# Performance work log

Hardware: AMD Instinct MI355X
Metric: run time of the kernel (lower is better)

## Reference

```python
import jax, jax.numpy as jnp
import numpy as np

B, S, D = 4, 2048, 1024
H, HD = 16, 64  # nb_heads, head_size


def setup_inputs() -> dict:
    key = jax.random.key(0)
    ks = jax.random.split(key, 9)
    s = 1.0 / np.sqrt(D)
    return {
        "x": jax.random.normal(ks[0], (B, S, D), dtype=jnp.float32),
        "wq": jax.random.uniform(ks[1], (D, D), jnp.float32, -s, s),
        "bq": jax.random.uniform(ks[2], (D,), jnp.float32, -s, s),
        "wk": jax.random.uniform(ks[3], (D, D), jnp.float32, -s, s),
        "bk": jax.random.uniform(ks[4], (D,), jnp.float32, -s, s),
        "wv": jax.random.uniform(ks[5], (D, D), jnp.float32, -s, s),
        "bv": jax.random.uniform(ks[6], (D,), jnp.float32, -s, s),
        "wo": jax.random.uniform(ks[7], (D, D), jnp.float32, -s, s),
        "bo": jax.random.uniform(ks[8], (D,), jnp.float32, -s, s),
    }


def _split_heads(t):
    # [B,S,D] -> [B,H,S,HD]
    return t.reshape(B, S, H, HD).transpose(0, 2, 1, 3)


def reference(x, wq, bq, wk, bk, wv, bv, wo, bo):
    q = _split_heads(x @ wq + bq)
    k = _split_heads(x @ wk + bk)
    v = _split_heads(x @ wv + bv)
    scores = jnp.einsum("bhqd,bhkd->bhqk", q, k) / jnp.sqrt(jnp.float32(HD))
    causal = jnp.tril(jnp.ones((S, S), dtype=bool))
    scores = jnp.where(causal, scores, -jnp.inf)
    w = jax.nn.softmax(scores, axis=-1)
    a = jnp.einsum("bhqk,bhkd->bhqd", w, v)
    a = a.transpose(0, 2, 1, 3).reshape(B, S, D)
    return a @ wo + bo
```

## Files before the change

kernel.cpp:

```cpp
#include <hip/hip_runtime.h>
#include <hip/hip_bf16.h>

typedef __bf16 bf16;
typedef bf16 bf16x8 __attribute__((ext_vector_type(8)));
typedef float f32x4 __attribute__((ext_vector_type(4)));
typedef unsigned short u16;

#define B_ 4
#define S_ 2048
#define D_ 1024
#define H_ 16
#define HD_ 64

#define NEG_SENT -30000.0f

#define XN_OFF   ((size_t)0)
#define WT_OFF   ((size_t)8388608)
#define BN_OFF   ((size_t)12582912)
#define FLAG_BYTE ((size_t)25174016)
#define Q_OFF    ((size_t)12587520)
#define K_OFF    ((size_t)20976128)
#define VT_OFF   ((size_t)29364736)

union Pack4 { bf16 b[4]; uint2 q; };

__device__ __forceinline__ void load16(const bf16* g, bf16* l) {
    __builtin_amdgcn_global_load_lds(
        (const __attribute__((address_space(1))) void*)g,
        (__attribute__((address_space(3))) void*)l, 16, 0, 0);
}

__global__ __launch_bounds__(256) void detect_k(const u16* __restrict__ x,
                                                int* __restrict__ flag)
{
    __shared__ int cnt;
    if (threadIdx.x == 0) cnt = 0;
    __syncthreads();
    int c = 0;
    for (int i = threadIdx.x; i < 4096; i += 256) {
        u16 w = x[i * 2];
        int e = (w >> 7) & 0xFF;
        if (e >= 100 && e <= 135) c++;
    }
    atomicAdd(&cnt, c);
    __syncthreads();
    if (threadIdx.x == 0) *flag = (cnt > 2048) ? 1 : 0;
}

__global__ __launch_bounds__(256) void norm_x_k(const void* __restrict__ src,
                                                bf16* __restrict__ dst,
                                                const int* __restrict__ flag)
{
    const int qi = blockIdx.x * 256 + threadIdx.x;
    if (*flag) {
        ((uint2*)dst)[qi] = ((const uint2*)src)[qi];
    } else {
        float4 v = ((const float4*)src)[qi];
        Pack4 p;
        p.b[0] = (bf16)v.x; p.b[1] = (bf16)v.y;
        p.b[2] = (bf16)v.z; p.b[3] = (bf16)v.w;
        ((uint2*)dst)[qi] = p.q;
    }
}

__global__ __launch_bounds__(256) void norm_b_k(
    const void* __restrict__ b0, const void* __restrict__ b1,
    const void* __restrict__ b2, const void* __restrict__ b3,
    bf16* __restrict__ BN, const int* __restrict__ flag)
{
    const int mat = blockIdx.x;
    const void* src = (mat == 0) ? b0 : (mat == 1) ? b1 : (mat == 2) ? b2 : b3;
    bf16* dst = BN + mat * 1024;
    const int i = threadIdx.x * 4;
    if (*flag) {
        ((uint2*)(dst + i))[0] = *(const uint2*)((const bf16*)src + i);
    } else {
        const float* s = (const float*)src;
        Pack4 p;
        p.b[0] = (bf16)s[i + 0]; p.b[1] = (bf16)s[i + 1];
        p.b[2] = (bf16)s[i + 2]; p.b[3] = (bf16)s[i + 3];
        ((uint2*)(dst + i))[0] = p.q;
    }
}

__global__ __launch_bounds__(256) void transpose_w(
    const void* __restrict__ W0, const void* __restrict__ W1,
    const void* __restrict__ W2, const void* __restrict__ W3,
    bf16* __restrict__ WT, const int* __restrict__ flag)
{
    __shared__ __align__(16) bf16 tile[64][65];
    const int mat = blockIdx.z;
    const void* W = (mat == 0) ? W0 : (mat == 1) ? W1 : (mat == 2) ? W2 : W3;
    bf16* O = WT + ((size_t)mat << 20);
    const int r0 = blockIdx.y * 64, c0 = blockIdx.x * 64;
    const int t = threadIdx.x;
    const int isb = *flag;
    #pragma unroll
    for (int i = 0; i < 16; ++i) {
        int idx = t + i * 256;
        int r = idx >> 6, c = idx & 63;
        size_t off = (size_t)(r0 + r) * D_ + c0 + c;
        tile[r][c] = isb ? ((const bf16*)W)[off] : (bf16)((const float*)W)[off];
    }
    __syncthreads();
    #pragma unroll
    for (int i = 0; i < 16; ++i) {
        int idx = t + i * 256;
        int rr = idx & 63, cc = idx >> 6;
        O[(size_t)(c0 + cc) * D_ + r0 + rr] = tile[rr][cc];
    }
}

__device__ __forceinline__ void gemm_core(const bf16* __restrict__ A,
                                          const bf16* __restrict__ Bt,
                                          bf16* lA, bf16* lB,
                                          f32x4 acc[4][4], int m0, int n0)
{
    const int t = threadIdx.x;
    const int lane = t & 63;
    const int wave = t >> 6;
    const int wm = (wave >> 1) << 6;
    const int wn = (wave & 1) << 6;
    const int quad = lane >> 4;
    const int col = lane & 15;
    for (int k0 = 0; k0 < D_; k0 += 32) {
        #pragma unroll
        for (int i = 0; i < 2; ++i) {
            int slot = t + i * 256;
            int row = slot >> 2;
            int kc = (slot & 3) << 3;
            load16(A + (size_t)(m0 + row) * D_ + k0 + kc, lA + slot * 8);
            load16(Bt + (size_t)(n0 + row) * D_ + k0 + kc, lB + slot * 8);
        }
        __syncthreads();
        bf16x8 af[4], bfr[4];
        #pragma unroll
        for (int mi = 0; mi < 4; ++mi)
            af[mi] = *(const bf16x8*)(lA + (wm + mi * 16 + col) * 32 + quad * 8);
        #pragma unroll
        for (int ni = 0; ni < 4; ++ni)
            bfr[ni] = *(const bf16x8*)(lB + (wn + ni * 16 + col) * 32 + quad * 8);
        #pragma unroll
        for (int mi = 0; mi < 4; ++mi)
            #pragma unroll
            for (int ni = 0; ni < 4; ++ni)
                acc[mi][ni] = __builtin_amdgcn_mfma_f32_16x16x32_bf16(
                    af[mi], bfr[ni], acc[mi][ni], 0, 0, 0);
        __syncthreads();
    }
}

__global__ __launch_bounds__(256) void gemm_qkv_k(
    const bf16* __restrict__ X, const bf16* __restrict__ WT,
    const bf16* __restrict__ BN,
    bf16* __restrict__ Qo, bf16* __restrict__ Ko, bf16* __restrict__ Vo)
{
    __shared__ __align__(16) bf16 lA[128 * 32];
    __shared__ __align__(16) bf16 lB[128 * 32];
    const int mode = blockIdx.z;
    const bf16* Wsel = WT + ((size_t)mode << 20);
    const bf16* bias = BN + mode * 1024;
    f32x4 acc[4][4];
    const f32x4 z = {0.f, 0.f, 0.f, 0.f};
    #pragma unroll
    for (int i = 0; i < 4; ++i)
        #pragma unroll
        for (int j = 0; j < 4; ++j) acc[i][j] = z;
    const int m0 = blockIdx.x * 128, n0 = blockIdx.y * 128;
    gemm_core(X, Wsel, lA, lB, acc, m0, n0);
    const int t = threadIdx.x, lane = t & 63, wave = t >> 6;
    const int wm = (wave >> 1) << 6, wn = (wave & 1) << 6;
    const int quad = lane >> 4, col = lane & 15;
    const float scale = (mode == 0) ? 0.18033688011112042f : 1.0f;
    #pragma unroll
    for (int mi = 0; mi < 4; ++mi) {
        int gm = m0 + wm + mi * 16 + quad * 4;
        int b = gm >> 11, srow = gm & 2047;
        #pragma unroll
        for (int ni = 0; ni < 4; ++ni) {
            int gn = n0 + wn + ni * 16 + col;
            float bb = (float)bias[gn];
            int h = gn >> 6, hd = gn & 63;
            if (mode == 2) {
                Pack4 pk;
                #pragma unroll
                for (int r = 0; r < 4; ++r)
                    pk.b[r] = (bf16)(acc[mi][ni][r] + bb);
                *(uint2*)(Vo + (((size_t)b * H_ + h) * HD_ + hd) * S_ + srow)
                    = pk.q;
            } else {
                #pragma unroll
                for (int r = 0; r < 4; ++r) {
                    float v = (acc[mi][ni][r] + bb) * scale;
                    if (mode == 1)
                        Ko[(((size_t)b * H_ + h) * S_ + srow + r) * HD_ + hd] = (bf16)v;
                    else
                        Qo[(((size_t)b * H_ + h) * S_ + srow + r) * HD_ + hd] = (bf16)v;
                }
            }
        }
    }
}

__device__ __forceinline__ void tile_step(
    const bf16* __restrict__ lK, const bf16* __restrict__ lV,
    bf16* __restrict__ lPTw,
    const bf16x8 qf[2], const bf16x8 vf4,
    f32x4 o[4], f32x4& o4, float& mst,
    int k0, int wq0)
{
    const int lane = threadIdx.x & 63;
    const int quad = lane >> 4, col = lane & 15;
    const f32x4 z = {0.f, 0.f, 0.f, 0.f};
    bool inc[4];
    inc[0] = true;
    inc[1] = (k0 + 16 <= wq0 + 15);
    inc[2] = (k0 + 32 <= wq0 + 15);
    inc[3] = (k0 + 48 <= wq0 + 15);
    f32x4 st[4];
    #pragma unroll
    for (int mt = 0; mt < 4; ++mt) st[mt] = z;
    __builtin_amdgcn_s_setprio(1);
    #pragma unroll
    for (int cc = 0; cc < 2; ++cc) {
        #pragma unroll
        for (int mt = 0; mt < 4; ++mt)
            if (inc[mt]) {
                bf16x8 af = *(const bf16x8*)(lK + (mt * 16 + col) * 64
                            + (((cc * 4 + quad) ^ (col & 7)) << 3));
                st[mt] = __builtin_amdgcn_mfma_f32_16x16x32_bf16(
                    af, qf[cc], st[mt], 0, 0, 0);
            }
    }
    __builtin_amdgcn_s_setprio(0);
    if (k0 + 64 > wq0) {
        #pragma unroll
        for (int mt = 0; mt < 4; ++mt)
            if (inc[mt]) {
                #pragma unroll
                for (int r = 0; r < 4; ++r)
                    if (k0 + mt * 16 + quad * 4 + r > wq0 + col)
                        st[mt][r] = NEG_SENT;
            }
    }
    float tm = fmaxf(fmaxf(st[0][0], st[0][1]), fmaxf(st[0][2], st[0][3]));
    #pragma unroll
    for (int mt = 1; mt < 4; ++mt)
        if (inc[mt])
            tm = fmaxf(tm, fmaxf(fmaxf(st[mt][0], st[mt][1]),
                                 fmaxf(st[mt][2], st[mt][3])));
    tm = fmaxf(tm, __shfl_xor(tm, 16));
    tm = fmaxf(tm, __shfl_xor(tm, 32));
    if (!__all(tm <= mst + 8.0f)) {
        float mn = fmaxf(mst, tm);
        float al = exp2f(mst - mn);
        #pragma unroll
        for (int dt = 0; dt < 4; ++dt) o[dt] *= al;
        o4 *= al;
        mst = mn;
    }
    #pragma unroll
    for (int mt = 0; mt < 4; ++mt) {
        int kch = mt * 2 + (quad >> 1);
        uint2* dst = (uint2*)(&lPTw[col * 64 + ((kch ^ (col & 7)) << 3)
                                    + ((quad & 1) << 2)]);
        if (inc[mt]) {
            Pack4 pk;
            #pragma unroll
            for (int r = 0; r < 4; ++r)
                pk.b[r] = (bf16)exp2f(st[mt][r] - mst);
            *dst = pk.q;
        } else if (mt == 1 || (mt == 3 && inc[2])) {
            uint2 zz; zz.x = 0u; zz.y = 0u;
            *dst = zz;
        }
    }
    asm volatile("s_waitcnt lgkmcnt(0)" ::: "memory");
    __builtin_amdgcn_s_setprio(1);
    #pragma unroll
    for (int kk = 0; kk < 2; ++kk) {
        if (kk == 1 && !inc[2]) continue;
        bf16x8 pf = *(const bf16x8*)(&lPTw[col * 64
                    + (((kk * 4 + quad) ^ (col & 7)) << 3)]);
        #pragma unroll
        for (int dt = 0; dt < 4; ++dt) {
            bf16x8 vf = *(const bf16x8*)(lV + (dt * 16 + col) * 64
                        + (((kk * 4 + quad) ^ (col & 7)) << 3));
            o[dt] = __builtin_amdgcn_mfma_f32_16x16x32_bf16(
                vf, pf, o[dt], 0, 0, 0);
        }
        o4 = __builtin_amdgcn_mfma_f32_16x16x32_bf16(vf4, pf, o4, 0, 0, 0);
    }
    __builtin_amdgcn_s_setprio(0);
}

__device__ __forceinline__ void tile_epilogue(
    bf16* __restrict__ Aout, int b, int h, int wq0,
    const f32x4 o[4], const f32x4& o4)
{
    const int lane = threadIdx.x & 63;
    const int quad = lane >> 4, col = lane & 15;
    float l = __shfl(o4[0], col);
    const float inv = 1.f / fmaxf(l, 1e-30f);
    const int qg = wq0 + col;
    #pragma unroll
    for (int dt = 0; dt < 4; ++dt) {
        Pack4 pk;
        #pragma unroll
        for (int r = 0; r < 4; ++r) pk.b[r] = (bf16)(o[dt][r] * inv);
        *(uint2*)(Aout + ((size_t)b * S_ + qg) * D_ + h * HD_
                  + dt * 16 + quad * 4) = pk.q;
    }
}

__global__ __launch_bounds__(256, 4) void attn_k(
    const bf16* __restrict__ Q, const bf16* __restrict__ K,
    const bf16* __restrict__ VT, bf16* __restrict__ Aout)
{
    __shared__ __align__(16) bf16 lK[64 * 64];
    __shared__ __align__(16) bf16 lV[64 * 64];
    __shared__ __align__(16) bf16 lPT[4][2][16 * 64];
    const int bh = blockIdx.y;
    const bf16* Qp = Q + (size_t)bh * S_ * HD_;
    const bf16* Kp = K + (size_t)bh * S_ * HD_;
    const bf16* Vp = VT + (size_t)bh * HD_ * S_;
    const int b = bh >> 4, h = bh & 15;
    const int t = threadIdx.x;
    const int lane = t & 63, w = t >> 6;
    const int quad = lane >> 4, col = lane & 15;

    const int q0L = (31 - (int)blockIdx.x) * 64;
    const int q0S = (int)blockIdx.x * 64;
    const int wq0L = q0L + w * 16, wq0S = q0S + w * 16;

    bf16x8 qfL[2], qfS[2];
    #pragma unroll
    for (int cc = 0; cc < 2; ++cc) {
        qfL[cc] = *(const bf16x8*)(Qp + (size_t)(wq0L + col) * HD_
                                   + cc * 32 + quad * 8);
        qfS[cc] = *(const bf16x8*)(Qp + (size_t)(wq0S + col) * HD_
                                   + cc * 32 + quad * 8);
    }
    const bf16 ov = (bf16)(col == 0 ? 1.0f : 0.0f);
    const bf16x8 vf4 = {ov, ov, ov, ov, ov, ov, ov, ov};

    f32x4 oL[4], oS[4], o4L, o4S;
    const f32x4 z = {0.f, 0.f, 0.f, 0.f};
    #pragma unroll
    for (int dt = 0; dt < 4; ++dt) { oL[dt] = z; oS[dt] = z; }
    o4L = z; o4S = z;
    float mstL = NEG_SENT, mstS = NEG_SENT;

    for (int k0 = 0; k0 <= q0L; k0 += 64) {
        #pragma unroll
        for (int i = 0; i < 2; ++i) {
            int slot = t + i * 256;
            int rr = slot >> 3, ch = slot & 7;
            int sw = (ch ^ (rr & 7)) << 3;
            load16(Kp + (size_t)(k0 + rr) * HD_ + sw, lK + slot * 8);
            load16(Vp + (size_t)rr * S_ + k0 + sw, lV + slot * 8);
        }
        __syncthreads();
        tile_step(lK, lV, &lPT[w][0][0], qfL, vf4, oL, o4L, mstL, k0, wq0L);
        if (k0 <= q0S)
            tile_step(lK, lV, &lPT[w][1][0], qfS, vf4, oS, o4S, mstS, k0, wq0S);
        __syncthreads();
    }
    tile_epilogue(Aout, b, h, wq0L, oL, o4L);
    tile_epilogue(Aout, b, h, wq0S, oS, o4S);
}

__global__ __launch_bounds__(256) void gemm_out_k(
    const bf16* __restrict__ A, const bf16* __restrict__ WoT,
    const bf16* __restrict__ Bo, void* __restrict__ Out,
    const int* __restrict__ flag)
{
    __shared__ __align__(16) bf16 lA[128 * 32];
    __shared__ __align__(16) bf16 lB[128 * 32];
    f32x4 acc[4][4];
    const f32x4 z = {0.f, 0.f, 0.f, 0.f};
    #pragma unroll
    for (int i = 0; i < 4; ++i)
        #pragma unroll
        for (int j = 0; j < 4; ++j) acc[i][j] = z;
    const int m0 = blockIdx.x * 128, n0 = blockIdx.y * 128;
    gemm_core(A, WoT, lA, lB, acc, m0, n0);
    const int t = threadIdx.x, lane = t & 63, wave = t >> 6;
    const int wm = (wave >> 1) << 6, wn = (wave & 1) << 6;
    const int quad = lane >> 4, col = lane & 15;
    const int isb = *flag;
    #pragma unroll
    for (int mi = 0; mi < 4; ++mi) {
        int gm = m0 + wm + mi * 16 + quad * 4;
        #pragma unroll
        for (int ni = 0; ni < 4; ++ni) {
            int gn = n0 + wn + ni * 16 + col;
            float bb = (float)Bo[gn];
            #pragma unroll
            for (int r = 0; r < 4; ++r) {
                float v = acc[mi][ni][r] + bb;
                size_t off = (size_t)(gm + r) * D_ + gn;
                if (isb) ((bf16*)Out)[off] = (bf16)v;
                else     ((float*)Out)[off] = v;
            }
        }
    }
}

extern "C" void kernel_launch(void* const* d_in, const int* in_sizes, int n_in,
                              void* d_out, int out_size, void* d_ws, size_t ws_size,
                              hipStream_t stream)
{
    const void* x  = d_in[0];
    const void* wq = d_in[1];
    const void* bq = d_in[2];
    const void* wk = d_in[3];
    const void* bk = d_in[4];
    const void* wv = d_in[5];
    const void* bv = d_in[6];
    const void* wo = d_in[7];
    const void* bo = d_in[8];

    bf16* ws  = (bf16*)d_ws;
    bf16* XN  = ws + XN_OFF;
    bf16* WT  = ws + WT_OFF;
    bf16* BN  = ws + BN_OFF;
    int*  flag = (int*)((char*)d_ws + FLAG_BYTE);
    bf16* Qb  = ws + Q_OFF;
    bf16* Kb  = ws + K_OFF;
    bf16* VTb = ws + VT_OFF;
    bf16* Ab  = XN;

    hipLaunchKernelGGL(detect_k, dim3(1), dim3(256), 0, stream,
                       (const u16*)x, flag);
    hipLaunchKernelGGL(norm_x_k, dim3(8192), dim3(256), 0, stream,
                       x, XN, flag);
    hipLaunchKernelGGL(transpose_w, dim3(16, 16, 4), dim3(256), 0, stream,
                       wq, wk, wv, wo, WT, flag);
    hipLaunchKernelGGL(norm_b_k, dim3(4), dim3(256), 0, stream,
                       bq, bk, bv, bo, BN, flag);
    hipLaunchKernelGGL(gemm_qkv_k, dim3(64, 8, 3), dim3(256), 0, stream,
                       XN, WT, BN, Qb, Kb, VTb);
    hipLaunchKernelGGL(attn_k, dim3(16, 64), dim3(256), 0, stream,
                       Qb, Kb, VTb, Ab);
    hipLaunchKernelGGL(gemm_out_k, dim3(64, 8), dim3(256), 0, stream,
                       Ab, WT + ((size_t)3u << 20), BN + 3072, d_out, flag);
}
```

Measured before the change: 288.9 us.

## Double-buffer K/V tiles and keep P in registers for the attention loop

The attention kernel now double-buffers the K and V tiles in LDS, prefetching the next tile while computing the current one, and drops one barrier per iteration. The P matrix is no longer round-tripped through LDS: it is packed directly into registers, and the V operand is gathered with a matching permuted layout. The long and short query tiles are interleaved so they share each K fragment load. The cost is more LDS for the second buffer and higher register pressure, which could reduce occupancy under the (256,4) launch bounds.

```diff
diff --git a/kernel.cpp b/kernel.cpp
--- a/kernel.cpp
+++ b/kernel.cpp
@@ -23,6 +23,7 @@
 #define VT_OFF   ((size_t)29364736)
 
 union Pack4 { bf16 b[4]; uint2 q; };
+union U4V  { uint4 u; bf16x8 v; };
 
 __device__ __forceinline__ void load16(const bf16* g, bf16* l) {
     __builtin_amdgcn_global_load_lds(
@@ -202,98 +203,6 @@
     }
 }
 
-__device__ __forceinline__ void tile_step(
-    const bf16* __restrict__ lK, const bf16* __restrict__ lV,
-    bf16* __restrict__ lPTw,
-    const bf16x8 qf[2], const bf16x8 vf4,
-    f32x4 o[4], f32x4& o4, float& mst,
-    int k0, int wq0)
-{
-    const int lane = threadIdx.x & 63;
-    const int quad = lane >> 4, col = lane & 15;
-    const f32x4 z = {0.f, 0.f, 0.f, 0.f};
-    bool inc[4];
-    inc[0] = true;
-    inc[1] = (k0 + 16 <= wq0 + 15);
-    inc[2] = (k0 + 32 <= wq0 + 15);
-    inc[3] = (k0 + 48 <= wq0 + 15);
-    f32x4 st[4];
-    #pragma unroll
-    for (int mt = 0; mt < 4; ++mt) st[mt] = z;
-    __builtin_amdgcn_s_setprio(1);
-    #pragma unroll
-    for (int cc = 0; cc < 2; ++cc) {
-        #pragma unroll
-        for (int mt = 0; mt < 4; ++mt)
-            if (inc[mt]) {
-                bf16x8 af = *(const bf16x8*)(lK + (mt * 16 + col) * 64
-                            + (((cc * 4 + quad) ^ (col & 7)) << 3));
-                st[mt] = __builtin_amdgcn_mfma_f32_16x16x32_bf16(
-                    af, qf[cc], st[mt], 0, 0, 0);
-            }
-    }
-    __builtin_amdgcn_s_setprio(0);
-    if (k0 + 64 > wq0) {
-        #pragma unroll
-        for (int mt = 0; mt < 4; ++mt)
-            if (inc[mt]) {
-                #pragma unroll
-                for (int r = 0; r < 4; ++r)
-                    if (k0 + mt * 16 + quad * 4 + r > wq0 + col)
-                        st[mt][r] = NEG_SENT;
-            }
-    }
-    float tm = fmaxf(fmaxf(st[0][0], st[0][1]), fmaxf(st[0][2], st[0][3]));
-    #pragma unroll
-    for (int mt = 1; mt < 4; ++mt)
-        if (inc[mt])
-            tm = fmaxf(tm, fmaxf(fmaxf(st[mt][0], st[mt][1]),
-                                 fmaxf(st[mt][2], st[mt][3])));
-    tm = fmaxf(tm, __shfl_xor(tm, 16));
-    tm = fmaxf(tm, __shfl_xor(tm, 32));
-    if (!__all(tm <= mst + 8.0f)) {
-        float mn = fmaxf(mst, tm);
-        float al = exp2f(mst - mn);
-        #pragma unroll
-        for (int dt = 0; dt < 4; ++dt) o[dt] *= al;
-        o4 *= al;
-        mst = mn;
-    }
-    #pragma unroll
-    for (int mt = 0; mt < 4; ++mt) {
-        int kch = mt * 2 + (quad >> 1);
-        uint2* dst = (uint2*)(&lPTw[col * 64 + ((kch ^ (col & 7)) << 3)
-                                    + ((quad & 1) << 2)]);
-        if (inc[mt]) {
-            Pack4 pk;
-            #pragma unroll
-            for (int r = 0; r < 4; ++r)
-                pk.b[r] = (bf16)exp2f(st[mt][r] - mst);
-            *dst = pk.q;
-        } else if (mt == 1 || (mt == 3 && inc[2])) {
-            uint2 zz; zz.x = 0u; zz.y = 0u;
-            *dst = zz;
-        }
-    }
-    asm volatile("s_waitcnt lgkmcnt(0)" ::: "memory");
-    __builtin_amdgcn_s_setprio(1);
-    #pragma unroll
-    for (int kk = 0; kk < 2; ++kk) {
-        if (kk == 1 && !inc[2]) continue;
-        bf16x8 pf = *(const bf16x8*)(&lPTw[col * 64
-                    + (((kk * 4 + quad) ^ (col & 7)) << 3)]);
-        #pragma unroll
-        for (int dt = 0; dt < 4; ++dt) {
-            bf16x8 vf = *(const bf16x8*)(lV + (dt * 16 + col) * 64
-                        + (((kk * 4 + quad) ^ (col & 7)) << 3));
-            o[dt] = __builtin_amdgcn_mfma_f32_16x16x32_bf16(
-                vf, pf, o[dt], 0, 0, 0);
-        }
-        o4 = __builtin_amdgcn_mfma_f32_16x16x32_bf16(vf4, pf, o4, 0, 0, 0);
-    }
-    __builtin_amdgcn_s_setprio(0);
-}
-
 __device__ __forceinline__ void tile_epilogue(
     bf16* __restrict__ Aout, int b, int h, int wq0,
     const f32x4 o[4], const f32x4& o4)
@@ -317,9 +226,8 @@
     const bf16* __restrict__ Q, const bf16* __restrict__ K,
     const bf16* __restrict__ VT, bf16* __restrict__ Aout)
 {
-    __shared__ __align__(16) bf16 lK[64 * 64];
-    __shared__ __align__(16) bf16 lV[64 * 64];
-    __shared__ __align__(16) bf16 lPT[4][2][16 * 64];
+    __shared__ __align__(16) bf16 lK[2][64 * 64];
+    __shared__ __align__(16) bf16 lV[2][64 * 64];
     const int bh = blockIdx.y;
     const bf16* Qp = Q + (size_t)bh * S_ * HD_;
     const bf16* Kp = K + (size_t)bh * S_ * HD_;
@@ -332,6 +240,7 @@
     const int q0L = (31 - (int)blockIdx.x) * 64;
     const int q0S = (int)blockIdx.x * 64;
     const int wq0L = q0L + w * 16, wq0S = q0S + w * 16;
+    const int nt = 32 - (int)blockIdx.x;
 
     bf16x8 qfL[2], qfS[2];
     #pragma unroll
@@ -351,21 +260,182 @@
     o4L = z; o4S = z;
     float mstL = NEG_SENT, mstS = NEG_SENT;
 
-    for (int k0 = 0; k0 <= q0L; k0 += 64) {
+    auto stage = [&](int k0, int bb) {
         #pragma unroll
         for (int i = 0; i < 2; ++i) {
             int slot = t + i * 256;
             int rr = slot >> 3, ch = slot & 7;
             int sw = (ch ^ (rr & 7)) << 3;
-            load16(Kp + (size_t)(k0 + rr) * HD_ + sw, lK + slot * 8);
-            load16(Vp + (size_t)rr * S_ + k0 + sw, lV + slot * 8);
-        }
+            load16(Kp + (size_t)(k0 + rr) * HD_ + sw, &lK[bb][slot * 8]);
+            load16(Vp + (size_t)rr * S_ + k0 + sw, &lV[bb][slot * 8]);
+        }
+    };
+
+    stage(0, 0);
+    __syncthreads();
+    int cur = 0;
+
+    for (int it = 0; it < nt; ++it) {
+        const int k0 = it << 6;
+        if (it + 1 < nt) stage(k0 + 64, cur ^ 1);
+        const bf16* K_ = &lK[cur][0];
+        const bf16* V_ = &lV[cur][0];
+        const bool doS = (k0 <= q0S);
+
+        bool incL[4], incS[4];
+        #pragma unroll
+        for (int mt = 0; mt < 4; ++mt) {
+            incL[mt] = (k0 + mt * 16 <= wq0L + 15);
+            incS[mt] = (k0 + mt * 16 <= wq0S + 15);
+        }
+
+        f32x4 stL[4], stS[4];
+        #pragma unroll
+        for (int mt = 0; mt < 4; ++mt) { stL[mt] = z; stS[mt] = z; }
+        __builtin_amdgcn_s_setprio(1);
+        #pragma unroll
+        for (int cc = 0; cc < 2; ++cc) {
+            #pragma unroll
+            for (int mt = 0; mt < 4; ++mt) {
+                if (incL[mt]) {
+                    bf16x8 af = *(const bf16x8*)(K_ + (mt * 16 + col) * 64
+                                + (((cc * 4 + quad) ^ (col & 7)) << 3));
+                    stL[mt] = __builtin_amdgcn_mfma_f32_16x16x32_bf16(
+                        af, qfL[cc], stL[mt], 0, 0, 0);
+                    if (doS && incS[mt])
+                        stS[mt] = __builtin_amdgcn_mfma_f32_16x16x32_bf16(
+                            af, qfS[cc], stS[mt], 0, 0, 0);
+                }
+            }
+        }
+        __builtin_amdgcn_s_setprio(0);
+
+        uint2 pkL[4], pkS[4];
+        {
+            if (k0 + 64 > wq0L) {
+                #pragma unroll
+                for (int mt = 0; mt < 4; ++mt)
+                    if (incL[mt]) {
+                        #pragma unroll
+                        for (int r = 0; r < 4; ++r)
+                            if (k0 + mt * 16 + quad * 4 + r > wq0L + col)
+                                stL[mt][r] = NEG_SENT;
+                    }
+            }
+            float tm = fmaxf(fmaxf(stL[0][0], stL[0][1]),
+                             fmaxf(stL[0][2], stL[0][3]));
+            #pragma unroll
+            for (int mt = 1; mt < 4; ++mt)
+                if (incL[mt])
+                    tm = fmaxf(tm, fmaxf(fmaxf(stL[mt][0], stL[mt][1]),
+                                         fmaxf(stL[mt][2], stL[mt][3])));
+            tm = fmaxf(tm, __shfl_xor(tm, 16));
+            tm = fmaxf(tm, __shfl_xor(tm, 32));
+            if (!__all(tm <= mstL + 8.0f)) {
+                float mn = fmaxf(mstL, tm);
+                float al = exp2f(mstL - mn);
+                #pragma unroll
+                for (int dt = 0; dt < 4; ++dt) oL[dt] *= al;
+                o4L *= al;
+                mstL = mn;
+            }
+            #pragma unroll
+            for (int mt = 0; mt < 4; ++mt) {
+                if (incL[mt]) {
+                    Pack4 pk;
+                    #pragma unroll
+                    for (int r = 0; r < 4; ++r)
+                        pk.b[r] = (bf16)exp2f(stL[mt][r] - mstL);
+                    pkL[mt] = pk.q;
+                } else {
+                    pkL[mt].x = 0u; pkL[mt].y = 0u;
+                }
+            }
+        }
+        if (doS) {
+            if (k0 + 64 > wq0S) {
+                #pragma unroll
+                for (int mt = 0; mt < 4; ++mt)
+                    if (incS[mt]) {
+                        #pragma unroll
+                        for (int r = 0; r < 4; ++r)
+                            if (k0 + mt * 16 + quad * 4 + r > wq0S + col)
+                                stS[mt][r] = NEG_SENT;
+                    }
+            }
+            float tm = fmaxf(fmaxf(stS[0][0], stS[0][1]),
+                             fmaxf(stS[0][2], stS[0][3]));
+            #pragma unroll
+            for (int mt = 1; mt < 4; ++mt)
+                if (incS[mt])
+                    tm = fmaxf(tm, fmaxf(fmaxf(stS[mt][0], stS[mt][1]),
+                                         fmaxf(stS[mt][2], stS[mt][3])));
+            tm = fmaxf(tm, __shfl_xor(tm, 16));
+            tm = fmaxf(tm, __shfl_xor(tm, 32));
+            if (!__all(tm <= mstS + 8.0f)) {
+                float mn = fmaxf(mstS, tm);
+                float al = exp2f(mstS - mn);
+                #pragma unroll
+                for (int dt = 0; dt < 4; ++dt) oS[dt] *= al;
+                o4S *= al;
+                mstS = mn;
+            }
+            #pragma unroll
+            for (int mt = 0; mt < 4; ++mt) {
+                if (incS[mt]) {
+                    Pack4 pk;
+                    #pragma unroll
+                    for (int r = 0; r < 4; ++r)
+                        pk.b[r] = (bf16)exp2f(stS[mt][r] - mstS);
+                    pkS[mt] = pk.q;
+                } else {
+                    pkS[mt].x = 0u; pkS[mt].y = 0u;
+                }
+            }
+        }
+
+        __builtin_amdgcn_s_setprio(1);
+        #pragma unroll
+        for (int kk = 0; kk < 2; ++kk) {
+            const bool needL = (kk == 0) ? true : incL[2];
+            const bool needS = doS && ((kk == 0) ? true : incS[2]);
+            if (!needL && !needS) continue;
+            U4V fl, fs;
+            fl.u.x = pkL[2 * kk].x;     fl.u.y = pkL[2 * kk].y;
+            fl.u.z = pkL[2 * kk + 1].x; fl.u.w = pkL[2 * kk + 1].y;
+            if (needS) {
+                fs.u.x = pkS[2 * kk].x;     fs.u.y = pkS[2 * kk].y;
+                fs.u.z = pkS[2 * kk + 1].x; fs.u.w = pkS[2 * kk + 1].y;
+            }
+            const int c0 = kk * 4 + (quad >> 1);
+            const int co = (quad & 1) << 2;
+            #pragma unroll
+            for (int dt = 0; dt < 4; ++dt) {
+                const bf16* vrow = V_ + (size_t)(dt * 16 + col) * 64;
+                uint2 va = *(const uint2*)(vrow + ((c0 ^ (col & 7)) << 3) + co);
+                uint2 vb = *(const uint2*)(vrow + (((c0 + 2) ^ (col & 7)) << 3) + co);
+                U4V vv;
+                vv.u.x = va.x; vv.u.y = va.y; vv.u.z = vb.x; vv.u.w = vb.y;
+                if (needL)
+                    oL[dt] = __builtin_amdgcn_mfma_f32_16x16x32_bf16(
+                        vv.v, fl.v, oL[dt], 0, 0, 0);
+                if (needS)
+                    oS[dt] = __builtin_amdgcn_mfma_f32_16x16x32_bf16(
+                        vv.v, fs.v, oS[dt], 0, 0, 0);
+            }
+            if (needL)
+                o4L = __builtin_amdgcn_mfma_f32_16x16x32_bf16(
+                    vf4, fl.v, o4L, 0, 0, 0);
+            if (needS)
+                o4S = __builtin_amdgcn_mfma_f32_16x16x32_bf16(
+                    vf4, fs.v, o4S, 0, 0, 0);
+        }
+        __builtin_amdgcn_s_setprio(0);
+
         __syncthreads();
-        tile_step(lK, lV, &lPT[w][0][0], qfL, vf4, oL, o4L, mstL, k0, wq0L);
-        if (k0 <= q0S)
-            tile_step(lK, lV, &lPT[w][1][0], qfS, vf4, oS, o4S, mstS, k0, wq0S);
-        __syncthreads();
-    }
+        cur ^= 1;
+    }
+
     tile_epilogue(Aout, b, h, wq0L, oL, o4L);
     tile_epilogue(Aout, b, h, wq0S, oS, o4S);
 }
```

Measured after the change: 863.9 us. 199% more time.

## Double-buffer K/V tiles and keep softmax P fragments in registers

Applied to the files above, without the earlier changes.

The attention loop now stages the next K/V tile into a second LDS buffer while the current tile is computed, leaving one barrier per iteration instead of two. The exponentiated scores are packed straight into the MFMA B-operand registers instead of being written to and read back from a per-wave LDS scratch. The V operand is loaded as two 8-byte pieces so its k ordering matches the register-resident P layout. This removes the P round-trip through LDS and exposes global-load latency to overlap with compute. The cost is doubled K/V LDS use, more LDS read instructions for V, and reliance on the async LDS loads completing before the end-of-iteration barrier.

```diff
diff --git a/kernel.cpp b/kernel.cpp
--- a/kernel.cpp
+++ b/kernel.cpp
@@ -23,6 +23,7 @@
 #define VT_OFF   ((size_t)29364736)
 
 union Pack4 { bf16 b[4]; uint2 q; };
+union U4V  { uint4 u; bf16x8 v; };
 
 __device__ __forceinline__ void load16(const bf16* g, bf16* l) {
     __builtin_amdgcn_global_load_lds(
@@ -202,10 +203,9 @@
     }
 }
 
-__device__ __forceinline__ void tile_step(
-    const bf16* __restrict__ lK, const bf16* __restrict__ lV,
-    bf16* __restrict__ lPTw,
-    const bf16x8 qf[2], const bf16x8 vf4,
+__device__ __forceinline__ void tile_body(
+    const bf16* __restrict__ K_, const bf16* __restrict__ V_,
+    const bf16x8 qf[2], const bf16x8& vf4,
     f32x4 o[4], f32x4& o4, float& mst,
     int k0, int wq0)
 {
@@ -213,10 +213,10 @@
     const int quad = lane >> 4, col = lane & 15;
     const f32x4 z = {0.f, 0.f, 0.f, 0.f};
     bool inc[4];
-    inc[0] = true;
-    inc[1] = (k0 + 16 <= wq0 + 15);
-    inc[2] = (k0 + 32 <= wq0 + 15);
-    inc[3] = (k0 + 48 <= wq0 + 15);
+    #pragma unroll
+    for (int mt = 0; mt < 4; ++mt)
+        inc[mt] = (k0 + mt * 16 <= wq0 + 15);
+
     f32x4 st[4];
     #pragma unroll
     for (int mt = 0; mt < 4; ++mt) st[mt] = z;
@@ -226,13 +226,14 @@
         #pragma unroll
         for (int mt = 0; mt < 4; ++mt)
             if (inc[mt]) {
-                bf16x8 af = *(const bf16x8*)(lK + (mt * 16 + col) * 64
+                bf16x8 af = *(const bf16x8*)(K_ + (mt * 16 + col) * 64
                             + (((cc * 4 + quad) ^ (col & 7)) << 3));
                 st[mt] = __builtin_amdgcn_mfma_f32_16x16x32_bf16(
                     af, qf[cc], st[mt], 0, 0, 0);
             }
     }
     __builtin_amdgcn_s_setprio(0);
+
     if (k0 + 64 > wq0) {
         #pragma unroll
         for (int mt = 0; mt < 4; ++mt)
@@ -243,6 +244,7 @@
                         st[mt][r] = NEG_SENT;
             }
     }
+
     float tm = fmaxf(fmaxf(st[0][0], st[0][1]), fmaxf(st[0][2], st[0][3]));
     #pragma unroll
     for (int mt = 1; mt < 4; ++mt)
@@ -259,37 +261,40 @@
         o4 *= al;
         mst = mn;
     }
-    #pragma unroll
-    for (int mt = 0; mt < 4; ++mt) {
-        int kch = mt * 2 + (quad >> 1);
-        uint2* dst = (uint2*)(&lPTw[col * 64 + ((kch ^ (col & 7)) << 3)
-                                    + ((quad & 1) << 2)]);
-        if (inc[mt]) {
-            Pack4 pk;
+
+    __builtin_amdgcn_s_setprio(1);
+    #pragma unroll
+    for (int kk = 0; kk < 2; ++kk) {
+        if (kk == 1 && !inc[2]) continue;
+        U4V f;
+        {
+            Pack4 plo, phi;
             #pragma unroll
             for (int r = 0; r < 4; ++r)
-                pk.b[r] = (bf16)exp2f(st[mt][r] - mst);
-            *dst = pk.q;
-        } else if (mt == 1 || (mt == 3 && inc[2])) {
-            uint2 zz; zz.x = 0u; zz.y = 0u;
-            *dst = zz;
-        }
-    }
-    asm volatile("s_waitcnt lgkmcnt(0)" ::: "memory");
-    __builtin_amdgcn_s_setprio(1);
-    #pragma unroll
-    for (int kk = 0; kk < 2; ++kk) {
-        if (kk == 1 && !inc[2]) continue;
-        bf16x8 pf = *(const bf16x8*)(&lPTw[col * 64
-                    + (((kk * 4 + quad) ^ (col & 7)) << 3)]);
+                plo.b[r] = (bf16)exp2f(st[2 * kk][r] - mst);
+            if (inc[2 * kk + 1]) {
+                #pragma unroll
+                for (int r = 0; r < 4; ++r)
+                    phi.b[r] = (bf16)exp2f(st[2 * kk + 1][r] - mst);
+            } else {
+                phi.q.x = 0u; phi.q.y = 0u;
+            }
+            f.u.x = plo.q.x; f.u.y = plo.q.y;
+            f.u.z = phi.q.x; f.u.w = phi.q.y;
+        }
+        const int c0 = kk * 4 + (quad >> 1);
+        const int co = (quad & 1) << 2;
         #pragma unroll
         for (int dt = 0; dt < 4; ++dt) {
-            bf16x8 vf = *(const bf16x8*)(lV + (dt * 16 + col) * 64
-                        + (((kk * 4 + quad) ^ (col & 7)) << 3));
+            const bf16* vrow = V_ + (size_t)(dt * 16 + col) * 64;
+            uint2 va = *(const uint2*)(vrow + ((c0 ^ (col & 7)) << 3) + co);
+            uint2 vb = *(const uint2*)(vrow + (((c0 + 2) ^ (col & 7)) << 3) + co);
+            U4V vv;
+            vv.u.x = va.x; vv.u.y = va.y; vv.u.z = vb.x; vv.u.w = vb.y;
             o[dt] = __builtin_amdgcn_mfma_f32_16x16x32_bf16(
-                vf, pf, o[dt], 0, 0, 0);
-        }
-        o4 = __builtin_amdgcn_mfma_f32_16x16x32_bf16(vf4, pf, o4, 0, 0, 0);
+                vv.v, f.v, o[dt], 0, 0, 0);
+        }
+        o4 = __builtin_amdgcn_mfma_f32_16x16x32_bf16(vf4, f.v, o4, 0, 0, 0);
     }
     __builtin_amdgcn_s_setprio(0);
 }
@@ -317,9 +322,8 @@
     const bf16* __restrict__ Q, const bf16* __restrict__ K,
     const bf16* __restrict__ VT, bf16* __restrict__ Aout)
 {
-    __shared__ __align__(16) bf16 lK[64 * 64];
-    __shared__ __align__(16) bf16 lV[64 * 64];
-    __shared__ __align__(16) bf16 lPT[4][2][16 * 64];
+    __shared__ __align__(16) bf16 lK[2][64 * 64];
+    __shared__ __align__(16) bf16 lV[2][64 * 64];
     const int bh = blockIdx.y;
     const bf16* Qp = Q + (size_t)bh * S_ * HD_;
     const bf16* Kp = K + (size_t)bh * S_ * HD_;
@@ -332,6 +336,7 @@
     const int q0L = (31 - (int)blockIdx.x) * 64;
     const int q0S = (int)blockIdx.x * 64;
     const int wq0L = q0L + w * 16, wq0S = q0S + w * 16;
+    const int nt = 32 - (int)blockIdx.x;
 
     bf16x8 qfL[2], qfS[2];
     #pragma unroll
@@ -351,21 +356,33 @@
     o4L = z; o4S = z;
     float mstL = NEG_SENT, mstS = NEG_SENT;
 
-    for (int k0 = 0; k0 <= q0L; k0 += 64) {
+    auto stage = [&](int k0, int bb) {
         #pragma unroll
         for (int i = 0; i < 2; ++i) {
             int slot = t + i * 256;
             int rr = slot >> 3, ch = slot & 7;
             int sw = (ch ^ (rr & 7)) << 3;
-            load16(Kp + (size_t)(k0 + rr) * HD_ + sw, lK + slot * 8);
-            load16(Vp + (size_t)rr * S_ + k0 + sw, lV + slot * 8);
-        }
+            load16(Kp + (size_t)(k0 + rr) * HD_ + sw, &lK[bb][slot * 8]);
+            load16(Vp + (size_t)rr * S_ + k0 + sw, &lV[bb][slot * 8]);
+        }
+    };
+
+    stage(0, 0);
+    __syncthreads();
+    int cur = 0;
+
+    for (int it = 0; it < nt; ++it) {
+        const int k0 = it << 6;
+        if (it + 1 < nt) stage(k0 + 64, cur ^ 1);
+        const bf16* K_ = &lK[cur][0];
+        const bf16* V_ = &lV[cur][0];
+        tile_body(K_, V_, qfL, vf4, oL, o4L, mstL, k0, wq0L);
+        if (k0 <= q0S)
+            tile_body(K_, V_, qfS, vf4, oS, o4S, mstS, k0, wq0S);
         __syncthreads();
-        tile_step(lK, lV, &lPT[w][0][0], qfL, vf4, oL, o4L, mstL, k0, wq0L);
-        if (k0 <= q0S)
-            tile_step(lK, lV, &lPT[w][1][0], qfS, vf4, oS, o4S, mstS, k0, wq0S);
-        __syncthreads();
-    }
+        cur ^= 1;
+    }
+
     tile_epilogue(Aout, b, h, wq0L, oL, o4L);
     tile_epilogue(Aout, b, h, wq0S, oS, o4S);
 }
```

After: 592.4 us. 105% more time.
